# Optimization experiments

Measured on AMD Instinct MI355X. Metric: run time of the kernel, lower is better.

## Reference

```python
import jax, jax.numpy as jnp
import numpy as np

D = 2048      # hidden_size
H = 16        # heads
HD = D // H   # head_dim = 128
FF = 8192     # intermediate_size
B = 4
S = 2048
FACTOR = 0.5  # mod_router_factor
EPS = 1e-6


def setup_inputs() -> dict:
    key = jax.random.key(0)
    ks = jax.random.split(key, 10)
    w = lambda k, shape: jax.random.normal(k, shape, jnp.float32) * 0.02
    return {
        "hidden_states": jax.random.normal(ks[0], (B, S, D), jnp.float32),
        "position_ids": jnp.arange(S, dtype=jnp.int32)[None, :],
        "mod_target_mask": jnp.ones((B, S), dtype=bool),
        "attention_mask_2d": jnp.ones((B, S), dtype=bool),
        "router_w": w(ks[1], (D,)),
        "ln1_w": jnp.ones((D,), jnp.float32),
        "ln2_w": jnp.ones((D,), jnp.float32),
        "Wq": w(ks[2], (D, D)),
        "Wk": w(ks[3], (D, D)),
        "Wv": w(ks[4], (D, D)),
        "Wo": w(ks[5], (D, D)),
        "W1": w(ks[6], (D, FF)),
        "W2": w(ks[7], (FF, D)),
    }


def _rmsnorm(x, w):
    return x * jax.lax.rsqrt(jnp.mean(x * x, axis=-1, keepdims=True) + EPS) * w


def _rope(x, pos):
    # x: [B,K,H,HD], pos: [B,K]
    half = HD // 2
    freqs = 1.0 / (10000.0 ** (jnp.arange(half, dtype=jnp.float32) / half))
    ang = pos[:, :, None].astype(jnp.float32) * freqs  # [B,K,half]
    cos = jnp.cos(ang)[:, :, None, :]
    sin = jnp.sin(ang)[:, :, None, :]
    x1, x2 = x[..., :half], x[..., half:]
    return jnp.concatenate([x1 * cos - x2 * sin, x2 * cos + x1 * sin], axis=-1)


def reference(hidden_states, position_ids, mod_target_mask, attention_mask_2d,
              router_w, ln1_w, ln2_w, Wq, Wk, Wv, Wo, W1, W2):
    Bq, Sq, _ = hidden_states.shape
    K = int(Sq * FACTOR)  # static top-k length (all rows fully mod-targeted)

    # --- token router ---
    logits = jnp.einsum('bsd,d->bs', hidden_states, router_w)
    logits = jnp.where(mod_target_mask, logits, -jnp.inf)
    weights = jax.nn.sigmoid(logits)  # weight_normalization: sigmoid * 1.0 + 0.0

    # --- top-k dispatch (indices sorted to preserve sequence order, matching
    # torch boolean-mask gather of kept tokens) ---
    _, idx = jax.lax.top_k(weights, K)
    idx = jnp.sort(idx, axis=1)                       # [B,K]
    bidx = jnp.arange(Bq)[:, None]
    kept = hidden_states[bidx, idx]                   # [B,K,D] residual
    pos = jnp.broadcast_to(position_ids, (Bq, Sq))[bidx, idx]

    # --- decoder layer (Llama-style pre-norm block) on kept tokens ---
    h1 = _rmsnorm(kept, ln1_w)
    q = _rope((h1 @ Wq).reshape(Bq, K, H, HD), pos)
    k = _rope((h1 @ Wk).reshape(Bq, K, H, HD), pos)
    v = (h1 @ Wv).reshape(Bq, K, H, HD)
    scores = jnp.einsum('bqhd,bkhd->bhqk', q, k) / np.sqrt(HD).astype(np.float32)
    causal = jnp.tril(jnp.ones((K, K), dtype=bool))
    scores = jnp.where(causal, scores, jnp.finfo(scores.dtype).min)
    attn = jax.nn.softmax(scores, axis=-1)
    ao = jnp.einsum('bhqk,bkhd->bqhd', attn, v).reshape(Bq, K, D) @ Wo
    h2 = kept + ao
    mlp = jax.nn.gelu(_rmsnorm(h2, ln2_w) @ W1) @ W2
    delta = ao + mlp  # forward_return_residual: layer_out - residual

    # --- combine: hidden[kept]=delta; hidden[target]*=w; hidden[kept]+=residual ---
    out = hidden_states.at[bidx, idx].set(delta)
    out = jnp.where(mod_target_mask[..., None], out * weights[..., None], out)
    out = out.at[bidx, idx].add(kept)
    return out
```

## Files before the change

kernel.cpp:

```cpp
#include <hip/hip_runtime.h>
#include <stdint.h>

#define Dm 2048
#define Hn 16
#define HDm 128
#define FFm 8192
#define Bm 4
#define Sm 2048
#define Km 1024

typedef __attribute__((ext_vector_type(4))) float f32x4;
typedef __attribute__((ext_vector_type(8))) short s16x8;
typedef unsigned short u16;
typedef unsigned int u32;

__device__ __forceinline__ float bf_lo(u32 u){ u32 x = u << 16; return __builtin_bit_cast(float, x); }
__device__ __forceinline__ float bf_hi(u32 u){ u32 x = u & 0xffff0000u; return __builtin_bit_cast(float, x); }
__device__ __forceinline__ float bfu(u16 u){ u32 x = ((u32)u) << 16; return __builtin_bit_cast(float, x); }
__device__ __forceinline__ u16 f2bf(float f){
  u32 u = __builtin_bit_cast(u32, f);
  u += 0x7fffu + ((u >> 16) & 1u);
  return (u16)(u >> 16);
}
__device__ __forceinline__ u32 pack2(float a, float b){
  return (u32)f2bf(a) | ((u32)f2bf(b) << 16);
}
__device__ __forceinline__ void unpack8(uint4 a, float* f){
  f[0]=bf_lo(a.x); f[1]=bf_hi(a.x); f[2]=bf_lo(a.y); f[3]=bf_hi(a.y);
  f[4]=bf_lo(a.z); f[5]=bf_hi(a.z); f[6]=bf_lo(a.w); f[7]=bf_hi(a.w);
}
__device__ __forceinline__ uint4 pack8(const float* f){
  uint4 o; o.x=pack2(f[0],f[1]); o.y=pack2(f[2],f[3]); o.z=pack2(f[4],f[5]); o.w=pack2(f[6],f[7]); return o;
}
__device__ __forceinline__ void load8_in(const void* p, size_t off, int fp32, float* f){
  if (fp32){
    const float* pf = (const float*)p + off;
    float4 a = *(const float4*)pf;
    float4 b = *(const float4*)(pf + 4);
    f[0]=a.x; f[1]=a.y; f[2]=a.z; f[3]=a.w;
    f[4]=b.x; f[5]=b.y; f[6]=b.z; f[7]=b.w;
  } else {
    uint4 a = *(const uint4*)((const u16*)p + off);
    unpack8(a, f);
  }
}
__device__ __forceinline__ float gelu_f(float x){
  float t = tanhf(0.7978845608028654f*(x + 0.044715f*x*x*x));
  return 0.5f*x*(1.0f + t);
}
__device__ __forceinline__ float block_sum256(float s){
  #pragma unroll
  for (int off = 32; off; off >>= 1) s += __shfl_xor(s, off);
  __shared__ float red[4];
  int lane = threadIdx.x & 63, w = threadIdx.x >> 6;
  if (lane == 0) red[w] = s;
  __syncthreads();
  return red[0] + red[1] + red[2] + red[3];
}
__device__ __forceinline__ void gload_lds16(const u16* g, u16* l){
  __builtin_amdgcn_global_load_lds((const __attribute__((address_space(1))) void*)g,
                                   (__attribute__((address_space(3))) void*)l, 16, 0, 0);
}

__global__ __launch_bounds__(256) void sniff_kernel(const u32* __restrict__ hs, int* __restrict__ flag){
  __shared__ int s;
  if (threadIdx.x == 0) s = 0;
  __syncthreads();
  int bad = 0;
  for (int i = threadIdx.x; i < 4096; i += 256){
    u32 w = hs[i];
    float lo = bf_lo(w), hi = bf_hi(w);
    if (!(fabsf(lo) < 1000.f && fabsf(hi) < 1000.f)) bad = 1;
  }
  if (bad) atomicOr(&s, 1);
  __syncthreads();
  if (threadIdx.x == 0) flag[0] = s;
}

__global__ __launch_bounds__(256) void router_kernel(const void* __restrict__ hs, const void* __restrict__ rw,
                                                     const int* __restrict__ dflag,
                                                     float* __restrict__ weights, int* __restrict__ selmap){
  int fp32 = *dflag;
  int row = blockIdx.x, t = threadIdx.x;
  float a[8], b8[8];
  load8_in(hs, (size_t)row*Dm + t*8, fp32, a);
  load8_in(rw, (size_t)t*8, fp32, b8);
  float s = 0.f;
  #pragma unroll
  for (int i = 0; i < 8; i++) s += a[i]*b8[i];
  float tot = block_sum256(s);
  if (t == 0){
    weights[row] = 1.0f/(1.0f + expf(-tot));
    selmap[row] = -1;
  }
}

__global__ __launch_bounds__(1024) void topk_kernel(const float* __restrict__ weights, const int* __restrict__ position_ids,
                                                    int* __restrict__ idx, int* __restrict__ pos, int* __restrict__ selmap){
  int b = blockIdx.x, t = threadIdx.x;
  __shared__ float v[Sm];
  __shared__ int id[Sm];
  v[t] = weights[b*Sm + t];             id[t] = t;
  v[t+1024] = weights[b*Sm + t + 1024]; id[t+1024] = t + 1024;
  for (int size = 2; size <= Sm; size <<= 1){
    for (int stride = size >> 1; stride > 0; stride >>= 1){
      __syncthreads();
      int lo = ((t & ~(stride-1)) << 1) | (t & (stride-1));
      int hi = lo + stride;
      bool up = (lo & size) == 0;
      float va = v[lo], vb = v[hi]; int ia = id[lo], ib = id[hi];
      bool aFirst = (va > vb) || (va == vb && ia < ib);
      if (up ? !aFirst : aFirst){ v[lo]=vb; v[hi]=va; id[lo]=ib; id[hi]=ia; }
    }
  }
  __syncthreads();
  for (int size = 2; size <= Km; size <<= 1){
    for (int stride = size >> 1; stride > 0; stride >>= 1){
      __syncthreads();
      if (t < Km/2){
        int lo = ((t & ~(stride-1)) << 1) | (t & (stride-1));
        int hi = lo + stride;
        bool up = (lo & size) == 0;
        int ia = id[lo], ib = id[hi];
        bool aFirst = ia < ib;
        if (up ? !aFirst : aFirst){ id[lo]=ib; id[hi]=ia; }
      }
    }
  }
  __syncthreads();
  if (t < Km){
    int iv = id[t];
    idx[b*Km + t] = iv;
    pos[b*Km + t] = position_ids[iv];
    selmap[b*Sm + iv] = t;
  }
}

__global__ __launch_bounds__(256) void gather_rmsnorm(const void* __restrict__ hs, const int* __restrict__ idx,
                                                      const void* __restrict__ ln1, const int* __restrict__ dflag,
                                                      u16* __restrict__ h1){
  int fp32 = *dflag;
  int g = blockIdx.x, t = threadIdx.x;
  int b = g >> 10;
  int row = idx[g];
  float f[8];
  load8_in(hs, ((size_t)b*Sm + row)*Dm + t*8, fp32, f);
  float ss = 0.f;
  #pragma unroll
  for (int i = 0; i < 8; i++) ss += f[i]*f[i];
  float tot = block_sum256(ss);
  float scale = rsqrtf(tot * (1.0f/Dm) + 1e-6f);
  float lw[8];
  load8_in(ln1, (size_t)t*8, fp32, lw);
  float o[8];
  #pragma unroll
  for (int i = 0; i < 8; i++) o[i] = f[i]*scale*lw[i];
  ((uint4*)(h1 + (size_t)g*Dm))[t] = pack8(o);
}

__global__ __launch_bounds__(256) void h2norm_kernel(const void* __restrict__ hs, const int* __restrict__ idx,
                                                     const u16* __restrict__ ao, const void* __restrict__ ln2,
                                                     const int* __restrict__ dflag, u16* __restrict__ h2n){
  int fp32 = *dflag;
  int g = blockIdx.x, t = threadIdx.x;
  int b = g >> 10;
  int row = idx[g];
  float ke[8], av[8];
  load8_in(hs, ((size_t)b*Sm + row)*Dm + t*8, fp32, ke);
  unpack8(((const uint4*)(ao + (size_t)g*Dm))[t], av);
  float f[8]; float ss = 0.f;
  #pragma unroll
  for (int i = 0; i < 8; i++){ f[i] = ke[i] + av[i]; ss += f[i]*f[i]; }
  float tot = block_sum256(ss);
  float scale = rsqrtf(tot * (1.0f/Dm) + 1e-6f);
  float lw[8];
  load8_in(ln2, (size_t)t*8, fp32, lw);
  float o[8];
  #pragma unroll
  for (int i = 0; i < 8; i++) o[i] = f[i]*scale*lw[i];
  ((uint4*)(h2n + (size_t)g*Dm))[t] = pack8(o);
}

__global__ __launch_bounds__(256) void transpose_k(const void* __restrict__ src, const int* __restrict__ dflag,
                                                   u16* __restrict__ dst, int R, int C, int ldS, size_t srcOff){
  int fp32 = *dflag;
  __shared__ u16 tile[64][72];
  int c0 = blockIdx.x << 6, r0 = blockIdx.y << 6;
  int t = threadIdx.x;
  int rr = t >> 3, cc = (t & 7) * 8;
  #pragma unroll
  for (int p = 0; p < 2; p++){
    float f[8];
    load8_in(src, srcOff + (size_t)(r0 + rr + p*32) * ldS + c0 + cc, fp32, f);
    u16 tmp[8];
    #pragma unroll
    for (int j = 0; j < 8; j++) tmp[j] = f2bf(f[j]);
    *(uint4*)&tile[rr + p*32][cc] = *(const uint4*)tmp;
  }
  __syncthreads();
  int col = t >> 3, r8 = (t & 7) * 8;
  #pragma unroll
  for (int p = 0; p < 2; p++){
    u16 tmp[8];
    #pragma unroll
    for (int j = 0; j < 8; j++) tmp[j] = tile[r8 + j][col + p*32];
    *(uint4*)(dst + (size_t)(c0 + col + p*32) * R + r0 + r8) = *(const uint4*)tmp;
  }
}

__global__ __launch_bounds__(256) void transpose_v(const u16* __restrict__ src, u16* __restrict__ dst){
  __shared__ u16 tile[64][72];
  int bh = blockIdx.z; int b = bh >> 4, h = bh & 15;
  int key0 = blockIdx.x << 6;
  int d0 = blockIdx.y << 6;
  int t = threadIdx.x;
  int rr = t >> 3, cc = (t & 7) * 8;
  #pragma unroll
  for (int p = 0; p < 2; p++){
    uint4 a = *(const uint4*)(src + ((size_t)(b*Km + key0 + rr + p*32))*Dm + h*HDm + d0 + cc);
    *(uint4*)&tile[rr + p*32][cc] = a;
  }
  __syncthreads();
  int col = t >> 3, r8 = (t & 7) * 8;
  #pragma unroll
  for (int p = 0; p < 2; p++){
    u16 tmp[8];
    #pragma unroll
    for (int j = 0; j < 8; j++) tmp[j] = tile[r8 + j][col + p*32];
    *(uint4*)(dst + ((size_t)bh*HDm + d0 + col + p*32)*Km + key0 + r8) = *(const uint4*)tmp;
  }
}

template<int BN>
__global__ __launch_bounds__(512, 2) void gemm256(const u16* __restrict__ A, const u16* __restrict__ BT,
                                                  u16* __restrict__ Cmat, int Kd, int lda, int ldb, int ldc,
                                                  int do_gelu, int accum){
  extern __shared__ u16 lds[];
  constexpr int WC    = BN / 4;
  constexpr int NREP  = BN / 64;
  constexpr int BTILE = BN * 64;
  constexpr int BROWS = BN / 8;
  constexpr int NSTGB = BN / 64;
  const int t    = threadIdx.x;
  const int lane = t & 63, wid = t >> 6;
  const int wr = wid >> 2, wc = wid & 3;
  const int l16 = lane & 15, quad = lane >> 4;
  const int m0 = blockIdx.x * 256, n0 = blockIdx.y * BN;

  const int lrow = lane >> 3;
  const int csw  = (lane & 7) ^ lrow;
  const u16* gA = A  + (size_t)(m0 + wid*32    + lrow) * lda + csw*8;
  const u16* gB = BT + (size_t)(n0 + wid*BROWS + lrow) * ldb + csw*8;

  f32x4 acc[8][NREP];
  #pragma unroll
  for (int i = 0; i < 8; i++)
    #pragma unroll
    for (int j = 0; j < NREP; j++) acc[i][j] = (f32x4){0.f,0.f,0.f,0.f};

  auto STAGE = [&](int buf, int kt){
    u16* la = lds + buf*16384 + (wid*32)*64;
    #pragma unroll
    for (int s = 0; s < 4; s++)
      gload_lds16(gA + (size_t)(s*8)*lda + kt*64, la + (s*8)*64);
    u16* lb = lds + 32768 + buf*BTILE + (wid*BROWS)*64;
    #pragma unroll
    for (int s = 0; s < NSTGB; s++)
      gload_lds16(gB + (size_t)(s*8)*ldb + kt*64, lb + (s*8)*64);
  };

  const int NT = Kd >> 6;
  STAGE(0, 0);
  for (int kt = 0; kt < NT; kt++){
    const int cur = kt & 1;
    if (kt + 1 < NT){
      STAGE(cur ^ 1, kt + 1);
      if constexpr (BN == 256) asm volatile("s_waitcnt vmcnt(8)" ::: "memory");
      else                     asm volatile("s_waitcnt vmcnt(6)" ::: "memory");
    } else {
      asm volatile("s_waitcnt vmcnt(0)" ::: "memory");
    }
    __builtin_amdgcn_s_barrier();
    __builtin_amdgcn_sched_barrier(0);
    const u16* LA = lds + cur*16384;
    const u16* LB = lds + 32768 + cur*BTILE;
    const int rsw = l16 & 7;
    s16x8 bf[NREP][2];
    #pragma unroll
    for (int ni = 0; ni < NREP; ni++)
      #pragma unroll
      for (int ks = 0; ks < 2; ks++)
        bf[ni][ks] = *(const s16x8*)(LB + (wc*WC + ni*16 + l16)*64 + ((ks*4 + quad) ^ rsw)*8);
    #pragma unroll
    for (int mi = 0; mi < 8; mi++){
      const u16* ar = LA + (wr*128 + mi*16 + l16)*64;
      s16x8 a0 = *(const s16x8*)(ar + ((quad     ^ rsw)*8));
      s16x8 a1 = *(const s16x8*)(ar + (((4+quad) ^ rsw)*8));
      __builtin_amdgcn_s_setprio(1);
      #pragma unroll
      for (int ni = 0; ni < NREP; ni++){
        acc[mi][ni] = __builtin_amdgcn_mfma_f32_16x16x32_bf16(a0, bf[ni][0], acc[mi][ni], 0, 0, 0);
        acc[mi][ni] = __builtin_amdgcn_mfma_f32_16x16x32_bf16(a1, bf[ni][1], acc[mi][ni], 0, 0, 0);
      }
      __builtin_amdgcn_s_setprio(0);
    }
    asm volatile("" ::: "memory");
    __builtin_amdgcn_s_barrier();
    __builtin_amdgcn_sched_barrier(0);
  }

  if (accum){
    #pragma unroll
    for (int mi = 0; mi < 8; mi++)
      #pragma unroll
      for (int ni = 0; ni < NREP; ni++){
        int rb = m0 + wr*128 + mi*16 + quad*4;
        int col = n0 + wc*WC + ni*16 + l16;
        #pragma unroll
        for (int r = 0; r < 4; r++){
          size_t off = (size_t)(rb + r)*ldc + col;
          float val = acc[mi][ni][r] + bfu(Cmat[off]);
          Cmat[off] = f2bf(val);
        }
      }
  } else {
    __syncthreads();
    u16* Ct = lds;
    #pragma unroll
    for (int mi = 0; mi < 8; mi++)
      #pragma unroll
      for (int ni = 0; ni < NREP; ni++){
        int rb = wr*128 + mi*16 + quad*4;
        int col = wc*WC + ni*16 + l16;
        #pragma unroll
        for (int r = 0; r < 4; r++){
          float v = acc[mi][ni][r];
          if (do_gelu) v = gelu_f(v);
          Ct[(rb + r)*BN + col] = f2bf(v);
        }
      }
    __syncthreads();
    constexpr int CH = (256*BN)/4096;
    #pragma unroll
    for (int i = 0; i < CH; i++){
      int off = i*4096 + t*8;
      int row = off / BN, col = off % BN;
      uint4 v = *(const uint4*)(Ct + off);
      *(uint4*)(Cmat + (size_t)(m0 + row)*ldc + n0 + col) = v;
    }
  }
}

__global__ __launch_bounds__(256) void rope_kernel(u16* __restrict__ qkb, const int* __restrict__ pos){
  int tid = blockIdx.x*256 + threadIdx.x;
  int row = tid >> 6, d = tid & 63;
  int grow = row >> 4, h = row & 15;
  float p = (float)pos[grow];
  float freq = exp2f(-0.20762050593589063f * (float)d);
  float ang = p * freq;
  float cs = cosf(ang), sn = sinf(ang);
  size_t base = (size_t)grow * 4096 + h*HDm + d;
  float x1 = bfu(qkb[base]), x2 = bfu(qkb[base+64]);
  qkb[base]    = f2bf(x1*cs - x2*sn);
  qkb[base+64] = f2bf(x2*cs + x1*sn);
  x1 = bfu(qkb[base+2048]); x2 = bfu(qkb[base+2048+64]);
  qkb[base+2048]    = f2bf(x1*cs - x2*sn);
  qkb[base+2048+64] = f2bf(x2*cs + x1*sn);
}

__global__ __launch_bounds__(256) void attn_mfma(const u16* __restrict__ qk, const u16* __restrict__ vt,
                                                 u16* __restrict__ o){
  __shared__ __align__(16) u16 Plds[4][32][40];
  const int w = threadIdx.x >> 6;
  const int lane = threadIdx.x & 63;
  const int l16 = lane & 15, quad = lane >> 4;
  const int bh = blockIdx.y;
  const int b = bh >> 4, h = bh & 15;
  const int bxr = (int)gridDim.x - 1 - (int)blockIdx.x;
  const int q0 = bxr * 128 + w * 32;
  const int QLD = 4096;

  s16x8 aq[2][4];
  #pragma unroll
  for (int qt = 0; qt < 2; qt++){
    const u16* qrow = qk + ((size_t)b*Km + q0 + qt*16 + l16)*QLD + h*HDm;
    #pragma unroll
    for (int kk = 0; kk < 4; kk++) aq[qt][kk] = *(const s16x8*)(qrow + kk*32 + quad*8);
  }
  const u16* kbase = qk + (size_t)b*Km*QLD + 2048 + h*HDm;
  const u16* vth   = vt + (size_t)bh * HDm * Km;

  f32x4 accO[2][8];
  #pragma unroll
  for (int qt = 0; qt < 2; qt++)
    #pragma unroll
    for (int n = 0; n < 8; n++) accO[qt][n] = (f32x4){0.f,0.f,0.f,0.f};
  float mrow[2][4], lrow[2][4];
  #pragma unroll
  for (int qt = 0; qt < 2; qt++)
    #pragma unroll
    for (int r = 0; r < 4; r++){ mrow[qt][r] = -1e30f; lrow[qt][r] = 0.f; }

  const float c = 0.08838834764831845f * 1.4426950408889634f;
  const int qmax = q0 + 31;

  for (int kt = 0; kt <= qmax; kt += 32){
    float sv[2][2][4];
    #pragma unroll
    for (int half = 0; half < 2; half++){
      s16x8 bk[4];
      const u16* krow = kbase + (size_t)(kt + half*16 + l16)*QLD;
      #pragma unroll
      for (int kk = 0; kk < 4; kk++) bk[kk] = *(const s16x8*)(krow + kk*32 + quad*8);
      int key = kt + half*16 + l16;
      #pragma unroll
      for (int qt = 0; qt < 2; qt++){
        f32x4 s = (f32x4){0.f,0.f,0.f,0.f};
        #pragma unroll
        for (int kk = 0; kk < 4; kk++)
          s = __builtin_amdgcn_mfma_f32_16x16x32_bf16(aq[qt][kk], bk[kk], s, 0, 0, 0);
        #pragma unroll
        for (int r = 0; r < 4; r++)
          sv[half][qt][r] = (key <= q0 + qt*16 + quad*4 + r) ? s[r]*c : -1e30f;
      }
    }
    float alpha[2][4];
    #pragma unroll
    for (int qt = 0; qt < 2; qt++){
      #pragma unroll
      for (int r = 0; r < 4; r++){
        float cm = fmaxf(sv[0][qt][r], sv[1][qt][r]);
        cm = fmaxf(cm, __shfl_xor(cm, 1));
        cm = fmaxf(cm, __shfl_xor(cm, 2));
        cm = fmaxf(cm, __shfl_xor(cm, 4));
        cm = fmaxf(cm, __shfl_xor(cm, 8));
        float mn = fmaxf(mrow[qt][r], cm);
        alpha[qt][r] = __builtin_amdgcn_exp2f(mrow[qt][r] - mn);
        mrow[qt][r] = mn;
        float p0 = __builtin_amdgcn_exp2f(sv[0][qt][r] - mn);
        float p1 = __builtin_amdgcn_exp2f(sv[1][qt][r] - mn);
        u16 u0 = f2bf(p0), u1 = f2bf(p1);
        Plds[w][qt*16 + quad*4 + r][l16]      = u0;
        Plds[w][qt*16 + quad*4 + r][16 + l16] = u1;
        float ps = bfu(u0) + bfu(u1);
        ps += __shfl_xor(ps, 1);
        ps += __shfl_xor(ps, 2);
        ps += __shfl_xor(ps, 4);
        ps += __shfl_xor(ps, 8);
        lrow[qt][r] = lrow[qt][r]*alpha[qt][r] + ps;
      }
    }
    asm volatile("s_waitcnt lgkmcnt(0)" ::: "memory");
    __builtin_amdgcn_sched_barrier(0);
    s16x8 ap[2];
    #pragma unroll
    for (int qt = 0; qt < 2; qt++) ap[qt] = *(const s16x8*)&Plds[w][qt*16 + l16][quad*8];
    #pragma unroll
    for (int qt = 0; qt < 2; qt++)
      #pragma unroll
      for (int n = 0; n < 8; n++)
        #pragma unroll
        for (int r = 0; r < 4; r++) accO[qt][n][r] *= alpha[qt][r];
    #pragma unroll
    for (int n = 0; n < 8; n++){
      s16x8 bv = *(const s16x8*)(vth + (size_t)(n*16 + l16)*Km + kt + quad*8);
      accO[0][n] = __builtin_amdgcn_mfma_f32_16x16x32_bf16(ap[0], bv, accO[0][n], 0, 0, 0);
      accO[1][n] = __builtin_amdgcn_mfma_f32_16x16x32_bf16(ap[1], bv, accO[1][n], 0, 0, 0);
    }
  }

  #pragma unroll
  for (int qt = 0; qt < 2; qt++){
    float inv[4];
    #pragma unroll
    for (int r = 0; r < 4; r++) inv[r] = 1.0f / lrow[qt][r];
    #pragma unroll
    for (int n = 0; n < 8; n++)
      #pragma unroll
      for (int r = 0; r < 4; r++){
        size_t off = ((size_t)b*Km + q0 + qt*16 + quad*4 + r)*Dm + h*HDm + n*16 + l16;
        o[off] = f2bf(accO[qt][n][r]*inv[r]);
      }
  }
}

__global__ __launch_bounds__(256) void final_kernel(const void* __restrict__ hidden, const float* __restrict__ weights,
                                                    const int* __restrict__ selmap, const u16* __restrict__ delta,
                                                    const int* __restrict__ dflag, void* __restrict__ outv){
  int fp32 = *dflag;
  int row = blockIdx.x, t = threadIdx.x;
  int b = row >> 11;
  float w = weights[row];
  int sel = selmap[row];
  float hv[8];
  load8_in(hidden, (size_t)row*Dm + t*8, fp32, hv);
  float f[8];
  if (sel >= 0){
    size_t ko = ((size_t)(b*Km + sel))*Dm;
    float dv[8];
    unpack8(((const uint4*)(delta+ko))[t], dv);
    #pragma unroll
    for (int i = 0; i < 8; i++) f[i] = dv[i]*w + hv[i];
  } else {
    #pragma unroll
    for (int i = 0; i < 8; i++) f[i] = hv[i]*w;
  }
  if (fp32){
    float* o = (float*)outv + (size_t)row*Dm + t*8;
    float4 x; x.x=f[0]; x.y=f[1]; x.z=f[2]; x.w=f[3];
    float4 y; y.x=f[4]; y.y=f[5]; y.z=f[6]; y.w=f[7];
    *(float4*)o = x; *(float4*)(o+4) = y;
  } else {
    ((uint4*)((u16*)outv + (size_t)row*Dm))[t] = pack8(f);
  }
}

extern "C" void kernel_launch(void* const* d_in, const int* in_sizes, int n_in,
                              void* d_out, int out_size, void* d_ws, size_t ws_size,
                              hipStream_t stream){
  (void)in_sizes; (void)n_in; (void)out_size; (void)ws_size;
  const void* hidden      = d_in[0];
  const int* position_ids = (const int*)d_in[1];
  const void* router_w = d_in[4];
  const void* ln1 = d_in[5];
  const void* ln2 = d_in[6];
  const void* Wq  = d_in[7];
  const void* Wk  = d_in[8];
  const void* Wv  = d_in[9];
  const void* Wo  = d_in[10];
  const void* W1  = d_in[11];
  const void* W2  = d_in[12];
  char* ws = (char*)d_ws;
  const size_t MB = 1ull << 20;
  float* weights = (float*)ws;
  int* idx     = (int*)(ws + 32768);
  int* pos     = (int*)(ws + 49152);
  int* selmap  = (int*)(ws + 65536);
  int* dflag   = (int*)(ws + 98304);
  u16* bufB  = (u16*)(ws +  1*MB);
  u16* qkbuf = (u16*)(ws + 17*MB);
  u16* aoB   = qkbuf;
  u16* TWbig = (u16*)(ws + 33*MB);
  u16* TW8   = (u16*)(ws + 49*MB);
  u16* vb   = (u16*)d_out;
  u16* TWqk = (u16*)d_out + 8ull*MB;
  u16* VT   = TWqk;
  u16* gbuf = (u16*)d_out;

  sniff_kernel<<<1, 256, 0, stream>>>((const u32*)hidden, dflag);
  router_kernel<<<Bm*Sm, 256, 0, stream>>>(hidden, router_w, dflag, weights, selmap);
  topk_kernel<<<Bm, 1024, 0, stream>>>(weights, position_ids, idx, pos, selmap);
  gather_rmsnorm<<<Bm*Km, 256, 0, stream>>>(hidden, idx, ln1, dflag, bufB);

  transpose_k<<<dim3(32,32), 256, 0, stream>>>(Wq, dflag, TWqk, Dm, Dm, Dm, 0);
  transpose_k<<<dim3(32,32), 256, 0, stream>>>(Wk, dflag, TWqk + (size_t)2048*2048, Dm, Dm, Dm, 0);
  gemm256<256><<<dim3(16,16), 512, 131072, stream>>>(bufB, TWqk, qkbuf, Dm, Dm, Dm, 4096, 0, 0);
  transpose_k<<<dim3(32,32), 256, 0, stream>>>(Wv, dflag, TW8, Dm, Dm, Dm, 0);
  gemm256<128><<<dim3(16,16), 512, 98304, stream>>>(bufB, TW8, vb, Dm, Dm, Dm, Dm, 0, 0);

  rope_kernel<<<16384, 256, 0, stream>>>(qkbuf, pos);
  transpose_v<<<dim3(16,2,64), 256, 0, stream>>>(vb, VT);
  attn_mfma<<<dim3(8,64), 256, 0, stream>>>(qkbuf, VT, bufB);

  transpose_k<<<dim3(32,32), 256, 0, stream>>>(Wo, dflag, TW8, Dm, Dm, Dm, 0);
  gemm256<128><<<dim3(16,16), 512, 98304, stream>>>(bufB, TW8, aoB, Dm, Dm, Dm, Dm, 0, 0);

  h2norm_kernel<<<Bm*Km, 256, 0, stream>>>(hidden, idx, aoB, ln2, dflag, bufB);

  for (int c = 0; c < 2; c++){
    transpose_k<<<dim3(64,32), 256, 0, stream>>>(W1, dflag, TWbig, Dm, 4096, FFm, (size_t)c*4096);
    gemm256<256><<<dim3(16,16), 512, 131072, stream>>>(bufB, TWbig, gbuf, Dm, Dm, Dm, 4096, 1, 0);
    transpose_k<<<dim3(32,64), 256, 0, stream>>>(W2, dflag, TWbig, 4096, Dm, Dm, (size_t)c*4096*Dm);
    gemm256<128><<<dim3(16,16), 512, 98304, stream>>>(gbuf, TWbig, aoB, 4096, 4096, 4096, Dm, 0, 1);
  }

  final_kernel<<<Bm*Sm, 256, 0, stream>>>(hidden, weights, selmap, aoB, dflag, d_out);
}
```

Measured before the change: 991.3 us.

## Stage accumulating GEMM epilogue through LDS and widen attention key tile

The accumulating GEMM epilogue now writes fp32 accumulators to shared memory, then does coalesced 16-byte read-modify-write of the bf16 output instead of scattered 2-byte accesses. Its dynamic LDS allocation is raised to fit the fp32 tile. The attention kernel processes 64 keys per iteration instead of 32, halving the online-softmax rescale and reduction overhead per key. In exchange it uses more registers and LDS, which could reduce occupancy.

Measured after the change: 961.4 us. 3.0% less time.

```diff
diff --git a/kernel.cpp b/kernel.cpp
--- a/kernel.cpp
+++ b/kernel.cpp
@@ -310,19 +310,32 @@
   }
 
   if (accum){
+    __syncthreads();
+    float* Cf = (float*)lds;
     #pragma unroll
     for (int mi = 0; mi < 8; mi++)
       #pragma unroll
       for (int ni = 0; ni < NREP; ni++){
-        int rb = m0 + wr*128 + mi*16 + quad*4;
-        int col = n0 + wc*WC + ni*16 + l16;
+        int rb = wr*128 + mi*16 + quad*4;
+        int col = wc*WC + ni*16 + l16;
         #pragma unroll
-        for (int r = 0; r < 4; r++){
-          size_t off = (size_t)(rb + r)*ldc + col;
-          float val = acc[mi][ni][r] + bfu(Cmat[off]);
-          Cmat[off] = f2bf(val);
-        }
+        for (int r = 0; r < 4; r++) Cf[(rb + r)*BN + col] = acc[mi][ni][r];
       }
+    __syncthreads();
+    constexpr int CH = (256*BN)/4096;
+    #pragma unroll
+    for (int i = 0; i < CH; i++){
+      int off = i*4096 + t*8;
+      int row = off / BN, col = off % BN;
+      u16* cp = Cmat + (size_t)(m0 + row)*ldc + n0 + col;
+      uint4 old = *(const uint4*)cp;
+      float f[8]; unpack8(old, f);
+      float4 a = *(const float4*)(Cf + off);
+      float4 b2 = *(const float4*)(Cf + off + 4);
+      float o[8] = {a.x+f[0], a.y+f[1], a.z+f[2], a.w+f[3],
+                    b2.x+f[4], b2.y+f[5], b2.z+f[6], b2.w+f[7]};
+      *(uint4*)cp = pack8(o);
+    }
   } else {
     __syncthreads();
     u16* Ct = lds;
@@ -370,7 +383,7 @@
 
 __global__ __launch_bounds__(256) void attn_mfma(const u16* __restrict__ qk, const u16* __restrict__ vt,
                                                  u16* __restrict__ o){
-  __shared__ __align__(16) u16 Plds[4][32][40];
+  __shared__ __align__(16) u16 Plds[4][32][72];
   const int w = threadIdx.x >> 6;
   const int lane = threadIdx.x & 63;
   const int l16 = lane & 15, quad = lane >> 4;
@@ -404,10 +417,10 @@
   const float c = 0.08838834764831845f * 1.4426950408889634f;
   const int qmax = q0 + 31;
 
-  for (int kt = 0; kt <= qmax; kt += 32){
-    float sv[2][2][4];
-    #pragma unroll
-    for (int half = 0; half < 2; half++){
+  for (int kt = 0; kt <= qmax; kt += 64){
+    float sv[4][2][4];
+    #pragma unroll
+    for (int half = 0; half < 4; half++){
       s16x8 bk[4];
       const u16* krow = kbase + (size_t)(kt + half*16 + l16)*QLD;
       #pragma unroll
@@ -429,7 +442,7 @@
     for (int qt = 0; qt < 2; qt++){
       #pragma unroll
       for (int r = 0; r < 4; r++){
-        float cm = fmaxf(sv[0][qt][r], sv[1][qt][r]);
+        float cm = fmaxf(fmaxf(sv[0][qt][r], sv[1][qt][r]), fmaxf(sv[2][qt][r], sv[3][qt][r]));
         cm = fmaxf(cm, __shfl_xor(cm, 1));
         cm = fmaxf(cm, __shfl_xor(cm, 2));
         cm = fmaxf(cm, __shfl_xor(cm, 4));
@@ -437,12 +450,14 @@
         float mn = fmaxf(mrow[qt][r], cm);
         alpha[qt][r] = __builtin_amdgcn_exp2f(mrow[qt][r] - mn);
         mrow[qt][r] = mn;
-        float p0 = __builtin_amdgcn_exp2f(sv[0][qt][r] - mn);
-        float p1 = __builtin_amdgcn_exp2f(sv[1][qt][r] - mn);
-        u16 u0 = f2bf(p0), u1 = f2bf(p1);
-        Plds[w][qt*16 + quad*4 + r][l16]      = u0;
-        Plds[w][qt*16 + quad*4 + r][16 + l16] = u1;
-        float ps = bfu(u0) + bfu(u1);
+        float ps = 0.f;
+        #pragma unroll
+        for (int hh = 0; hh < 4; hh++){
+          float p = __builtin_amdgcn_exp2f(sv[hh][qt][r] - mn);
+          u16 u = f2bf(p);
+          Plds[w][qt*16 + quad*4 + r][hh*16 + l16] = u;
+          ps += bfu(u);
+        }
         ps += __shfl_xor(ps, 1);
         ps += __shfl_xor(ps, 2);
         ps += __shfl_xor(ps, 4);
@@ -452,9 +467,12 @@
     }
     asm volatile("s_waitcnt lgkmcnt(0)" ::: "memory");
     __builtin_amdgcn_sched_barrier(0);
-    s16x8 ap[2];
-    #pragma unroll
-    for (int qt = 0; qt < 2; qt++) ap[qt] = *(const s16x8*)&Plds[w][qt*16 + l16][quad*8];
+    s16x8 ap[2][2];
+    #pragma unroll
+    for (int qt = 0; qt < 2; qt++){
+      ap[qt][0] = *(const s16x8*)&Plds[w][qt*16 + l16][quad*8];
+      ap[qt][1] = *(const s16x8*)&Plds[w][qt*16 + l16][32 + quad*8];
+    }
     #pragma unroll
     for (int qt = 0; qt < 2; qt++)
       #pragma unroll
@@ -463,9 +481,13 @@
         for (int r = 0; r < 4; r++) accO[qt][n][r] *= alpha[qt][r];
     #pragma unroll
     for (int n = 0; n < 8; n++){
-      s16x8 bv = *(const s16x8*)(vth + (size_t)(n*16 + l16)*Km + kt + quad*8);
-      accO[0][n] = __builtin_amdgcn_mfma_f32_16x16x32_bf16(ap[0], bv, accO[0][n], 0, 0, 0);
-      accO[1][n] = __builtin_amdgcn_mfma_f32_16x16x32_bf16(ap[1], bv, accO[1][n], 0, 0, 0);
+      const u16* vrow = vth + (size_t)(n*16 + l16)*Km + kt;
+      s16x8 bv0 = *(const s16x8*)(vrow + quad*8);
+      s16x8 bv1 = *(const s16x8*)(vrow + 32 + quad*8);
+      accO[0][n] = __builtin_amdgcn_mfma_f32_16x16x32_bf16(ap[0][0], bv0, accO[0][n], 0, 0, 0);
+      accO[0][n] = __builtin_amdgcn_mfma_f32_16x16x32_bf16(ap[0][1], bv1, accO[0][n], 0, 0, 0);
+      accO[1][n] = __builtin_amdgcn_mfma_f32_16x16x32_bf16(ap[1][0], bv0, accO[1][n], 0, 0, 0);
+      accO[1][n] = __builtin_amdgcn_mfma_f32_16x16x32_bf16(ap[1][1], bv1, accO[1][n], 0, 0, 0);
     }
   }
 
@@ -571,7 +593,7 @@
     transpose_k<<<dim3(64,32), 256, 0, stream>>>(W1, dflag, TWbig, Dm, 4096, FFm, (size_t)c*4096);
     gemm256<256><<<dim3(16,16), 512, 131072, stream>>>(bufB, TWbig, gbuf, Dm, Dm, Dm, 4096, 1, 0);
     transpose_k<<<dim3(32,64), 256, 0, stream>>>(W2, dflag, TWbig, 4096, Dm, Dm, (size_t)c*4096*Dm);
-    gemm256<128><<<dim3(16,16), 512, 98304, stream>>>(gbuf, TWbig, aoB, 4096, 4096, 4096, Dm, 0, 1);
+    gemm256<128><<<dim3(16,16), 512, 131072, stream>>>(gbuf, TWbig, aoB, 4096, 4096, 4096, Dm, 0, 1);
   }
 
   final_kernel<<<Bm*Sm, 256, 0, stream>>>(hidden, weights, selmap, aoB, dflag, d_out);
```
